# Performance work log

Measured on AMD Instinct MI355X. Metric: run time of the kernel, lower is better.

Reference implementation:

```python
import jax, jax.numpy as jnp
import numpy as np

B, C_IN, C_OUT, N = 16, 256, 256, 1024


def setup_inputs() -> dict:
    key = jax.random.key(0)
    k1, k2, k3, k4, k5 = jax.random.split(key, 5)
    x = jax.random.normal(k1, (B, C_IN, N), dtype=jnp.float32)
    adj1 = jax.random.uniform(k2, (B, N, N), dtype=jnp.float32)
    adj2 = jax.random.uniform(k3, (B, N, N), dtype=jnp.float32)
    # weight init: normal(0, 0.01) as in reset_parameters
    weight = jax.random.normal(k4, (C_OUT, C_IN), dtype=jnp.float32) * 0.01
    stdv = 1.0 / np.sqrt(C_IN)
    bias = jax.random.uniform(k5, (1, C_OUT, 1), minval=-stdv, maxval=stdv, dtype=jnp.float32)
    return {"x": x, "adj1": adj1, "adj2": adj2, "weight": weight, "bias": bias}


def reference(x, adj1, adj2, weight, bias):
    half = weight.shape[0] // 2
    # per-sample chained matmul: W_half @ (x_i @ A_i), batched
    xa1 = jnp.einsum('bcn,bnm->bcm', x, adj1)          # [B, C_in, N]
    xa2 = jnp.einsum('bcn,bnm->bcm', x, adj2)          # [B, C_in, N]
    out1 = jnp.einsum('oc,bcm->bom', weight[:half], xa1)  # [B, C_out/2, N]
    out2 = jnp.einsum('oc,bcm->bom', weight[half:], xa2)  # [B, C_out/2, N]
    out = jnp.concatenate([out1, out2], axis=1) + bias     # [B, C_out, N]
    return jax.nn.relu(out)
```

## Files before the change

### kernel.cpp

```cpp
#include <hip/hip_runtime.h>
#include <hip/hip_bf16.h>

typedef unsigned short u16;
typedef unsigned int u32;
typedef __attribute__((ext_vector_type(8))) short bf16x8;
typedef __attribute__((ext_vector_type(4))) float f32x4;

__device__ __forceinline__ u16 f2bf(float f) {
  return __builtin_bit_cast(u16, __float2bfloat16(f));
}

__device__ __forceinline__ bf16x8 ld_frag16(const u16* p) {
  return __builtin_bit_cast(bf16x8, *reinterpret_cast<const uint4*>(p));
}

__device__ __forceinline__ void gload_lds16(const void* g, void* l) {
  __builtin_amdgcn_global_load_lds((const __attribute__((address_space(1))) void*)g,
                                   (__attribute__((address_space(3))) void*)l, 16, 0, 0);
}

__device__ __forceinline__ void bar_lds() {
  asm volatile("s_waitcnt lgkmcnt(0)" ::: "memory");
  __builtin_amdgcn_sched_barrier(0);
  __builtin_amdgcn_s_barrier();
}

__global__ __launch_bounds__(256, 3) void gemm1(
    const float* __restrict__ x, const float* __restrict__ weight,
    u16* __restrict__ Y)
{
  constexpr int Nn = 1024, K = 256, BK = 32, SB = 40;
  __shared__ __align__(16) u16 As[128 * 32];
  __shared__ __align__(16) u16 Bs[64 * SB];

  const int t = threadIdx.x;
  const int b = blockIdx.z, mt = blockIdx.y, n0 = blockIdx.x * 64;

  const float* Wp = weight + (size_t)mt * 128 * K;
  const float* Xb = x + (size_t)b * K * Nn;

  const int w = t >> 6, l = t & 63;
  const int wm = w >> 1, wn = w & 1;
  const int lr = l & 15, lg = l >> 4;

  const int ar = t >> 1, akc = (t & 1) * 16;
  const int bm = t & 63, bkq = t >> 6;
  const float* Xcol = Xb + n0 + bm;

  f32x4 acc[4][2] = {};

  for (int kt = 0; kt < K / BK; ++kt) {
    const int k0 = kt * BK;

    float4 a4[4];
#pragma unroll
    for (int uu = 0; uu < 4; ++uu)
      a4[uu] = reinterpret_cast<const float4*>(Wp + (size_t)ar * K + k0 + akc)[uu];
    union { uint4 q[2]; u16 s[16]; } ua;
#pragma unroll
    for (int uu = 0; uu < 4; ++uu) {
      ua.s[uu * 4 + 0] = f2bf(a4[uu].x); ua.s[uu * 4 + 1] = f2bf(a4[uu].y);
      ua.s[uu * 4 + 2] = f2bf(a4[uu].z); ua.s[uu * 4 + 3] = f2bf(a4[uu].w);
    }
    {
      const int c0 = akc >> 3;
      const int sw = (ar >> 1) & 3;
      uint4* Aq = reinterpret_cast<uint4*>(As);
      Aq[ar * 4 + ((c0 + 0) ^ sw)] = ua.q[0];
      Aq[ar * 4 + ((c0 + 1) ^ sw)] = ua.q[1];
    }

    float v[8];
#pragma unroll
    for (int j = 0; j < 8; ++j)
      v[j] = Xcol[(size_t)(k0 + bkq * 8 + j) * Nn];
    union { uint4 q; u16 s[8]; } ub;
#pragma unroll
    for (int j = 0; j < 8; ++j) ub.s[j] = f2bf(v[j]);
    reinterpret_cast<uint4*>(Bs)[bm * 5 + bkq] = ub.q;

    __syncthreads();

    bf16x8 af[4], bfr[2];
#pragma unroll
    for (int mi = 0; mi < 4; ++mi) {
      const int rr = wm * 64 + mi * 16 + lr;
      const int cw = lg ^ ((rr >> 1) & 3);
      af[mi] = ld_frag16(As + rr * BK + cw * 8);
    }
#pragma unroll
    for (int ni = 0; ni < 2; ++ni) {
      const int cc = wn * 32 + ni * 16 + lr;
      bfr[ni] = ld_frag16(Bs + cc * SB + lg * 8);
    }
#pragma unroll
    for (int mi = 0; mi < 4; ++mi)
#pragma unroll
      for (int ni = 0; ni < 2; ++ni)
        acc[mi][ni] = __builtin_amdgcn_mfma_f32_16x16x32_bf16(
            af[mi], bfr[ni], acc[mi][ni], 0, 0, 0);

    __syncthreads();
  }

#pragma unroll
  for (int mi = 0; mi < 4; ++mi) {
#pragma unroll
    for (int rr = 0; rr < 4; ++rr) {
      const int row = mt * 128 + wm * 64 + mi * 16 + lg * 4 + rr;
      u16* Yrow = Y + ((size_t)(b * 256 + row)) * Nn + n0;
#pragma unroll
      for (int ni = 0; ni < 2; ++ni) {
        const int col = wn * 32 + ni * 16 + lr;
        Yrow[col] = f2bf(acc[mi][ni][rr]);
      }
    }
  }
}

__global__ __launch_bounds__(512, 4) void gemm2(
    const float* __restrict__ adj1, const float* __restrict__ adj2,
    const u16* __restrict__ Y, const float* __restrict__ bias,
    float* __restrict__ out)
{
  constexpr int Nn = 1024, BK = 32, SB = 40, NT = Nn / BK;
  __shared__ __align__(16) u16 As[4][128 * 32];
  __shared__ __align__(16) u16 Bs[4][64 * SB];

  const int t = threadIdx.x;
  const int b = blockIdx.z, h = blockIdx.y, n0 = blockIdx.x * 64;

  const float* adj = (h == 0 ? adj1 : adj2) + (size_t)b * Nn * Nn;
  const u16* Yb = Y + ((size_t)(b * 256 + h * 128)) * Nn;

  const int w = t >> 6, l = t & 63;
  const int wm = w >> 1, wn = w & 1;
  const int lr = l & 15, lg = l >> 4;

  const int a_r = t >> 2, a_c = t & 3;
  const int a_cg = a_c ^ ((a_r >> 1) & 3);
  const u16* a_src = Yb + (size_t)a_r * Nn + a_cg * 8;
  const int a_dstoff = (w * 64) * 8;

  const int bm = l, bkq = w;
  const float* adjcol = adj + n0 + bm;
  const int b_dstoff = bm * SB + bkq * 4;

  f32x4 acc[2][2] = {};

  auto ISSUE_A = [&](int tt) {
    gload_lds16(a_src + tt * BK, (void*)(&As[tt & 3][0] + a_dstoff));
  };
  auto LOAD_B = [&](int tt, float* v) {
#pragma unroll
    for (int j = 0; j < 4; ++j)
      v[j] = adjcol[(size_t)(tt * BK + bkq * 4 + j) * Nn];
  };
  auto WRITE_B = [&](int tt, const float* v) {
    union { uint2 q; u16 s[4]; } ub;
#pragma unroll
    for (int j = 0; j < 4; ++j) ub.s[j] = f2bf(v[j]);
    *reinterpret_cast<uint2*>(&Bs[tt & 3][0] + b_dstoff) = ub.q;
  };
  auto COMPUTE = [&](int tt) {
    const u16* Ab = &As[tt & 3][0];
    const u16* Bb = &Bs[tt & 3][0];
    bf16x8 af[2], bfr[2];
#pragma unroll
    for (int mi = 0; mi < 2; ++mi) {
      const int rr = wm * 32 + mi * 16 + lr;
      const int cw = lg ^ ((rr >> 1) & 3);
      af[mi] = ld_frag16(Ab + rr * BK + cw * 8);
    }
#pragma unroll
    for (int ni = 0; ni < 2; ++ni) {
      const int cc = wn * 32 + ni * 16 + lr;
      bfr[ni] = ld_frag16(Bb + cc * SB + lg * 8);
    }
#pragma unroll
    for (int mi = 0; mi < 2; ++mi)
#pragma unroll
      for (int ni = 0; ni < 2; ++ni)
        acc[mi][ni] = __builtin_amdgcn_mfma_f32_16x16x32_bf16(
            af[mi], bfr[ni], acc[mi][ni], 0, 0, 0);
  };

  float vA[4], vB[4];

  ISSUE_A(0); LOAD_B(0, vA);
  ISSUE_A(1); LOAD_B(1, vB);
  WRITE_B(0, vA);
  bar_lds();

  for (int jj = 0; jj < NT / 2; ++jj) {
    const int j0 = 2 * jj;
    if (j0 + 2 < NT) { ISSUE_A(j0 + 2); LOAD_B(j0 + 2, vA); }
    WRITE_B(j0 + 1, vB);
    COMPUTE(j0);
    bar_lds();
    const int j1 = j0 + 1;
    if (j1 + 2 < NT) { ISSUE_A(j1 + 2); LOAD_B(j1 + 2, vB); }
    if (j1 + 1 < NT) WRITE_B(j1 + 1, vA);
    COMPUTE(j1);
    if (jj != NT / 2 - 1) bar_lds();
  }

#pragma unroll
  for (int mi = 0; mi < 2; ++mi) {
#pragma unroll
    for (int rr = 0; rr < 4; ++rr) {
      const int go = h * 128 + wm * 32 + mi * 16 + lg * 4 + rr;
      const float bi = bias[go];
      float* orow = out + ((size_t)(b * 256 + go)) * Nn + n0;
#pragma unroll
      for (int ni = 0; ni < 2; ++ni) {
        const int col = wn * 32 + ni * 16 + lr;
        orow[col] = fmaxf(acc[mi][ni][rr] + bi, 0.f);
      }
    }
  }
}

extern "C" void kernel_launch(void* const* d_in, const int* in_sizes, int n_in,
                              void* d_out, int out_size, void* d_ws, size_t ws_size,
                              hipStream_t stream) {
  const float* x    = (const float*)d_in[0];
  const float* adj1 = (const float*)d_in[1];
  const float* adj2 = (const float*)d_in[2];
  const float* wgt  = (const float*)d_in[3];
  const float* bias = (const float*)d_in[4];
  float* out = (float*)d_out;
  u16* Y = (u16*)d_ws;

  dim3 g1(16, 2, 16);
  gemm1<<<g1, dim3(256), 0, stream>>>(x, wgt, Y);
  dim3 g2(16, 2, 16);
  gemm2<<<g2, dim3(512), 0, stream>>>(adj1, adj2, Y, bias, out);
}
```

Before: 52.24 us.

## Widen gemm2 column tile and load adjacency rows as float4 with LDS transpose

The second GEMM's column tile grows from 64 to 128. Each warp now computes a 64x32 output block, so the grid is halved and the launch bounds change. The adjacency tile is loaded with row-wise float4 loads, converted to bf16 into a row-major staging buffer, then transposed through LDS in a second pass into the column-major layout the MFMA fragments expect. This aims for wider, more efficient global loads of the large adjacency matrices and more reuse of each Y tile per block. The cost is an extra LDS transpose pass per k-step and only 256 blocks, which means lower occupancy and a weaker ability to hide latency.

```diff
diff --git a/kernel.cpp b/kernel.cpp
--- a/kernel.cpp
+++ b/kernel.cpp
@@ -118,23 +118,26 @@
   }
 }
 
-__global__ __launch_bounds__(512, 4) void gemm2(
+__global__ __launch_bounds__(512, 2) void gemm2(
     const float* __restrict__ adj1, const float* __restrict__ adj2,
     const u16* __restrict__ Y, const float* __restrict__ bias,
     float* __restrict__ out)
 {
-  constexpr int Nn = 1024, BK = 32, SB = 40, NT = Nn / BK;
+  constexpr int Nn = 1024, BK = 32, NT = Nn / BK;
+  constexpr int SB1 = 132;
+  constexpr int SB2 = 40;
   __shared__ __align__(16) u16 As[4][128 * 32];
-  __shared__ __align__(16) u16 Bs[4][64 * SB];
+  __shared__ __align__(16) u16 Bb[2][32 * SB1];
+  __shared__ __align__(16) u16 Bs2[2][128 * SB2];
 
   const int t = threadIdx.x;
-  const int b = blockIdx.z, h = blockIdx.y, n0 = blockIdx.x * 64;
+  const int b = blockIdx.z, h = blockIdx.y, n0 = blockIdx.x * 128;
 
   const float* adj = (h == 0 ? adj1 : adj2) + (size_t)b * Nn * Nn;
   const u16* Yb = Y + ((size_t)(b * 256 + h * 128)) * Nn;
 
   const int w = t >> 6, l = t & 63;
-  const int wm = w >> 1, wn = w & 1;
+  const int wm = w >> 2, wn = w & 3;
   const int lr = l & 15, lg = l >> 4;
 
   const int a_r = t >> 2, a_c = t & 3;
@@ -142,74 +145,89 @@
   const u16* a_src = Yb + (size_t)a_r * Nn + a_cg * 8;
   const int a_dstoff = (w * 64) * 8;
 
-  const int bm = l, bkq = w;
-  const float* adjcol = adj + n0 + bm;
-  const int b_dstoff = bm * SB + bkq * 4;
-
-  f32x4 acc[2][2] = {};
+  const int b1r = t >> 5, b1c4 = t & 31;
+  const float* bsrc0 = adj + (size_t)(0 * 16 + b1r) * Nn + n0 + 4 * b1c4;
+  const float* bsrc1 = adj + (size_t)(1 * 16 + b1r) * Nn + n0 + 4 * b1c4;
+
+  const int p2n = t >> 2, p2kq = t & 3;
+
+  f32x4 acc[4][2] = {};
 
   auto ISSUE_A = [&](int tt) {
     gload_lds16(a_src + tt * BK, (void*)(&As[tt & 3][0] + a_dstoff));
   };
-  auto LOAD_B = [&](int tt, float* v) {
-#pragma unroll
-    for (int j = 0; j < 4; ++j)
-      v[j] = adjcol[(size_t)(tt * BK + bkq * 4 + j) * Nn];
-  };
-  auto WRITE_B = [&](int tt, const float* v) {
-    union { uint2 q; u16 s[4]; } ub;
-#pragma unroll
-    for (int j = 0; j < 4; ++j) ub.s[j] = f2bf(v[j]);
-    *reinterpret_cast<uint2*>(&Bs[tt & 3][0] + b_dstoff) = ub.q;
+  auto LOAD_B = [&](int tt, float4* v) {
+    v[0] = *reinterpret_cast<const float4*>(bsrc0 + (size_t)tt * BK * Nn);
+    v[1] = *reinterpret_cast<const float4*>(bsrc1 + (size_t)tt * BK * Nn);
+  };
+  auto PASS1 = [&](int tt, const float4* v) {
+#pragma unroll
+    for (int i = 0; i < 2; ++i) {
+      union { uint2 q; u16 s[4]; } ub;
+      ub.s[0] = f2bf(v[i].x); ub.s[1] = f2bf(v[i].y);
+      ub.s[2] = f2bf(v[i].z); ub.s[3] = f2bf(v[i].w);
+      *reinterpret_cast<uint2*>(&Bb[tt & 1][0] + (i * 16 + b1r) * SB1 + 4 * b1c4) = ub.q;
+    }
+  };
+  auto PASS2 = [&](int tt) {
+    const u16* src = &Bb[tt & 1][0];
+    union { uint4 q; u16 s[8]; } up;
+#pragma unroll
+    for (int j2 = 0; j2 < 8; ++j2)
+      up.s[j2] = src[(p2kq * 8 + j2) * SB1 + p2n];
+    *reinterpret_cast<uint4*>(&Bs2[tt & 1][0] + p2n * SB2 + p2kq * 8) = up.q;
   };
   auto COMPUTE = [&](int tt) {
     const u16* Ab = &As[tt & 3][0];
-    const u16* Bb = &Bs[tt & 3][0];
-    bf16x8 af[2], bfr[2];
-#pragma unroll
-    for (int mi = 0; mi < 2; ++mi) {
-      const int rr = wm * 32 + mi * 16 + lr;
+    const u16* Bbf = &Bs2[tt & 1][0];
+    bf16x8 af[4], bfr[2];
+#pragma unroll
+    for (int mi = 0; mi < 4; ++mi) {
+      const int rr = wm * 64 + mi * 16 + lr;
       const int cw = lg ^ ((rr >> 1) & 3);
       af[mi] = ld_frag16(Ab + rr * BK + cw * 8);
     }
 #pragma unroll
     for (int ni = 0; ni < 2; ++ni) {
       const int cc = wn * 32 + ni * 16 + lr;
-      bfr[ni] = ld_frag16(Bb + cc * SB + lg * 8);
-    }
-#pragma unroll
-    for (int mi = 0; mi < 2; ++mi)
+      bfr[ni] = ld_frag16(Bbf + cc * SB2 + lg * 8);
+    }
+#pragma unroll
+    for (int mi = 0; mi < 4; ++mi)
 #pragma unroll
       for (int ni = 0; ni < 2; ++ni)
         acc[mi][ni] = __builtin_amdgcn_mfma_f32_16x16x32_bf16(
             af[mi], bfr[ni], acc[mi][ni], 0, 0, 0);
   };
 
-  float vA[4], vB[4];
-
-  ISSUE_A(0); LOAD_B(0, vA);
-  ISSUE_A(1); LOAD_B(1, vB);
-  WRITE_B(0, vA);
+  float4 regA[2], regB[2];
+
+  ISSUE_A(0); LOAD_B(0, regA);
+  ISSUE_A(1); LOAD_B(1, regB);
+  PASS1(0, regA);
   bar_lds();
 
   for (int jj = 0; jj < NT / 2; ++jj) {
     const int j0 = 2 * jj;
-    if (j0 + 2 < NT) { ISSUE_A(j0 + 2); LOAD_B(j0 + 2, vA); }
-    WRITE_B(j0 + 1, vB);
+    if (j0 + 2 < NT) { ISSUE_A(j0 + 2); LOAD_B(j0 + 2, regA); }
+    PASS1(j0 + 1, regB);
+    PASS2(j0);
+    bar_lds();
     COMPUTE(j0);
+
+    const int j1 = j0 + 1;
+    if (j1 + 2 < NT) { ISSUE_A(j1 + 2); LOAD_B(j1 + 2, regB); }
+    if (j1 + 1 < NT) PASS1(j1 + 1, regA);
+    PASS2(j1);
     bar_lds();
-    const int j1 = j0 + 1;
-    if (j1 + 2 < NT) { ISSUE_A(j1 + 2); LOAD_B(j1 + 2, vB); }
-    if (j1 + 1 < NT) WRITE_B(j1 + 1, vA);
     COMPUTE(j1);
-    if (jj != NT / 2 - 1) bar_lds();
-  }
-
-#pragma unroll
-  for (int mi = 0; mi < 2; ++mi) {
+  }
+
+#pragma unroll
+  for (int mi = 0; mi < 4; ++mi) {
 #pragma unroll
     for (int rr = 0; rr < 4; ++rr) {
-      const int go = h * 128 + wm * 32 + mi * 16 + lg * 4 + rr;
+      const int go = h * 128 + wm * 64 + mi * 16 + lg * 4 + rr;
       const float bi = bias[go];
       float* orow = out + ((size_t)(b * 256 + go)) * Nn + n0;
 #pragma unroll
@@ -234,6 +252,6 @@
 
   dim3 g1(16, 2, 16);
   gemm1<<<g1, dim3(256), 0, stream>>>(x, wgt, Y);
-  dim3 g2(16, 2, 16);
+  dim3 g2(8, 2, 16);
   gemm2<<<g2, dim3(512), 0, stream>>>(adj1, adj2, Y, bias, out);
 }
```

Result: no change. 52.75 us (+1.0%).
